# Kernel tuning notes

Hardware: AMD Instinct MI355X
Metric: run time of the kernel (lower is better)

## Reference

```python
import jax, jax.numpy as jnp
import numpy as np

B, T, C, H, HS, L, V, BITS = 4, 512, 768, 12, 64, 12, 50257, 16


def _ln(x, g, b, eps=1e-5):
    m = x.mean(-1, keepdims=True)
    v = ((x - m) ** 2).mean(-1, keepdims=True)
    return (x - m) * jax.lax.rsqrt(v + eps) * g + b


def setup_inputs() -> dict:
    key = jax.random.key(0)
    ks = jax.random.split(key, 12)
    s = 0.02
    return {
        "idx": jax.random.randint(ks[0], (B, T), 0, V),
        "tok_emb": jax.random.normal(ks[1], (V, C), jnp.float32) * s,
        "pos_emb": jax.random.normal(ks[2], (T, C), jnp.float32) * s,
        "Wq": jax.random.normal(ks[3], (L, H, C, HS), jnp.float32) * s,
        "Wk": jax.random.normal(ks[4], (L, H, C, HS), jnp.float32) * s,
        "Wv": jax.random.normal(ks[5], (L, H, C, HS), jnp.float32) * s,
        "Wo": jax.random.normal(ks[6], (L, C, C), jnp.float32) * s,
        "bo": jnp.zeros((L, C), jnp.float32),
        "W1": jax.random.normal(ks[7], (L, C, 4 * C), jnp.float32) * s,
        "b1": jnp.zeros((L, 4 * C), jnp.float32),
        "W2": jax.random.normal(ks[8], (L, 4 * C, C), jnp.float32) * s,
        "b2": jnp.zeros((L, C), jnp.float32),
        "ln1_g": jnp.ones((L, C), jnp.float32),
        "ln1_b": jnp.zeros((L, C), jnp.float32),
        "ln2_g": jnp.ones((L, C), jnp.float32),
        "ln2_b": jnp.zeros((L, C), jnp.float32),
        "lnf_g": jnp.ones((C,), jnp.float32),
        "lnf_b": jnp.zeros((C,), jnp.float32),
        "Wh": jax.random.normal(ks[9], (C, BITS), jnp.float32) * s,
        "bh": jnp.zeros((BITS,), jnp.float32),
    }


def reference(idx, tok_emb, pos_emb, Wq, Wk, Wv, Wo, bo, W1, b1, W2, b2,
              ln1_g, ln1_b, ln2_g, ln2_b, lnf_g, lnf_b, Wh, bh):
    Bc, Tc = idx.shape
    x = tok_emb[idx] + pos_emb[:Tc]          # [B,T,C]
    mask = jnp.tril(jnp.ones((Tc, Tc), bool))  # causal tril buffer
    scale = HS ** -0.5

    def block(x, p):
        wq, wk, wv, wo, bo_, w1, b1_, w2, b2_, g1, bb1, g2, bb2 = p
        xn = _ln(x, g1, bb1)
        q = jnp.einsum('btc,hcd->bhtd', xn, wq)
        k = jnp.einsum('btc,hcd->bhtd', xn, wk)
        v = jnp.einsum('btc,hcd->bhtd', xn, wv)
        wei = jnp.einsum('bhtd,bhsd->bhts', q, k) * scale
        wei = jnp.where(mask, wei, -jnp.inf)
        wei = jax.nn.softmax(wei, axis=-1)
        o = jnp.einsum('bhts,bhsd->bhtd', wei, v)
        o = o.transpose(0, 2, 1, 3).reshape(Bc, Tc, H * HS)  # concat heads
        x = x + o @ wo + bo_
        xn2 = _ln(x, g2, bb2)
        h = jax.nn.gelu(xn2 @ w1 + b1_, approximate=False)  # exact GELU (torch default)
        x = x + h @ w2 + b2_
        return x, None

    x, _ = jax.lax.scan(block, x, (Wq, Wk, Wv, Wo, bo, W1, b1, W2, b2,
                                   ln1_g, ln1_b, ln2_g, ln2_b))
    x = _ln(x, lnf_g, lnf_b)
    logits = x @ Wh + bh                      # [B,T,16] ECOC logits
    return logits
```

## Files before the change

kernel.cpp:

```cpp
#include <hip/hip_runtime.h>
#include <hip/hip_bf16.h>
#include <math.h>

#define TT   512
#define CC   768
#define HH   12
#define HSZ  64
#define LL   12
#define C4   3072
#define BTOT 2048
#define NQKV 2304
#define NX   ((long)BTOT * CC)

typedef __attribute__((ext_vector_type(8))) short short8;
typedef __attribute__((ext_vector_type(4))) float f32x4;

__device__ __forceinline__ unsigned short f2b_bits(float f) {
    unsigned u = __float_as_uint(f);
    return (unsigned short)((u + 0x7fffu + ((u >> 16) & 1u)) >> 16);
}
__device__ __forceinline__ float b2f(unsigned short b) {
    return __uint_as_float((unsigned)b << 16);
}

__device__ __forceinline__ void gl_lds16(const void* g, void* l) {
    __builtin_amdgcn_global_load_lds(
        (const __attribute__((address_space(1))) unsigned int*)g,
        (__attribute__((address_space(3))) unsigned int*)l,
        16, 0, 0);
}

__global__ __launch_bounds__(256) void embed_k(const int* __restrict__ idx,
    const float* __restrict__ tok, const float* __restrict__ pos,
    float* __restrict__ x)
{
    int r   = blockIdx.x;
    int tid = threadIdx.x;
    int t   = r & (TT - 1);
    long id = idx[r];
    const float* te = tok + id * (long)CC;
    const float* pe = pos + (long)t * CC;
    float* xr = x + (long)r * CC;
#pragma unroll
    for (int i = 0; i < 3; ++i) {
        int c = tid + i * 256;
        xr[c] = te[c] + pe[c];
    }
}

__global__ __launch_bounds__(256) void ln_b(const float* __restrict__ x,
    const float* __restrict__ g, const float* __restrict__ b,
    __hip_bfloat16* __restrict__ y)
{
    int r = blockIdx.x, tid = threadIdx.x;
    const float* xr = x + (long)r * CC;
    float v[3];
    v[0] = xr[tid]; v[1] = xr[tid + 256]; v[2] = xr[tid + 512];
    float s  = v[0] + v[1] + v[2];
    float sq = v[0]*v[0] + v[1]*v[1] + v[2]*v[2];
#pragma unroll
    for (int off = 32; off > 0; off >>= 1) {
        s  += __shfl_down(s, off);
        sq += __shfl_down(sq, off);
    }
    __shared__ float ss[4], ssq[4];
    int w = tid >> 6;
    if ((tid & 63) == 0) { ss[w] = s; ssq[w] = sq; }
    __syncthreads();
    s  = ss[0] + ss[1] + ss[2] + ss[3];
    sq = ssq[0] + ssq[1] + ssq[2] + ssq[3];
    float mean = s * (1.0f / CC);
    float var  = sq * (1.0f / CC) - mean * mean;
    float rs   = rsqrtf(var + 1e-5f);
    __hip_bfloat16* yr = y + (long)r * CC;
#pragma unroll
    for (int i = 0; i < 3; ++i) {
        int c = tid + i * 256;
        yr[c] = __float2bfloat16((v[i] - mean) * rs * g[c] + b[c]);
    }
}

template <bool DOLN>
__global__ __launch_bounds__(256) void red_ln(float* __restrict__ x,
    const unsigned short* __restrict__ p, const float* __restrict__ bias,
    const float* __restrict__ g, const float* __restrict__ b,
    __hip_bfloat16* __restrict__ y)
{
    int r = blockIdx.x, tid = threadIdx.x;
    float* xr = x + (long)r * CC;
    const unsigned short* pr = p + (long)r * CC;
    float v[3];
#pragma unroll
    for (int i = 0; i < 3; ++i) {
        int c = tid + i * 256;
        float s = xr[c] + bias[c];
        s += b2f(pr[c]);
        s += b2f(pr[c + 1 * NX]);
        s += b2f(pr[c + 2 * NX]);
        s += b2f(pr[c + 3 * NX]);
        xr[c] = s;
        v[i] = s;
    }
    if (!DOLN) return;
    float s  = v[0] + v[1] + v[2];
    float sq = v[0]*v[0] + v[1]*v[1] + v[2]*v[2];
#pragma unroll
    for (int off = 32; off > 0; off >>= 1) {
        s  += __shfl_down(s, off);
        sq += __shfl_down(sq, off);
    }
    __shared__ float ss[4], ssq[4];
    int w = tid >> 6;
    if ((tid & 63) == 0) { ss[w] = s; ssq[w] = sq; }
    __syncthreads();
    s  = ss[0] + ss[1] + ss[2] + ss[3];
    sq = ssq[0] + ssq[1] + ssq[2] + ssq[3];
    float mean = s * (1.0f / CC);
    float var  = sq * (1.0f / CC) - mean * mean;
    float rs   = rsqrtf(var + 1e-5f);
    __hip_bfloat16* yr = y + (long)r * CC;
#pragma unroll
    for (int i = 0; i < 3; ++i) {
        int c = tid + i * 256;
        yr[c] = __float2bfloat16((v[i] - mean) * rs * g[c] + b[c]);
    }
}

__global__ __launch_bounds__(256) void cvtT_k(const float* __restrict__ src,
    __hip_bfloat16* __restrict__ dst, int R, int D, long sSrc, long sDst)
{
    src += (long)blockIdx.z * sSrc;
    dst += (long)blockIdx.z * sDst;
    __shared__ float t[64][65];
    int d0 = blockIdx.x * 64, r0 = blockIdx.y * 64;
    int tid = threadIdx.x;
#pragma unroll
    for (int i = 0; i < 4; ++i) {
        int flat = tid + i * 256;
        int r = flat >> 4, c4 = (flat & 15) * 4;
        float4 v = *(const float4*)&src[(long)(r0 + r) * D + d0 + c4];
        t[r][c4 + 0] = v.x; t[r][c4 + 1] = v.y;
        t[r][c4 + 2] = v.z; t[r][c4 + 3] = v.w;
    }
    __syncthreads();
#pragma unroll
    for (int i = 0; i < 4; ++i) {
        int flat = tid + i * 256;
        int n = flat >> 4, kq = (flat & 15) * 4;
        ushort4 o;
        o.x = f2b_bits(t[kq + 0][n]); o.y = f2b_bits(t[kq + 1][n]);
        o.z = f2b_bits(t[kq + 2][n]); o.w = f2b_bits(t[kq + 3][n]);
        *(ushort4*)&dst[(long)(d0 + n) * R + r0 + kq] = o;
    }
}

__global__ __launch_bounds__(256) void cvt_qkvT(const float* __restrict__ Wq,
    const float* __restrict__ Wk, const float* __restrict__ Wv,
    __hip_bfloat16* __restrict__ out)
{
    int c0 = blockIdx.x * 64;
    int g  = blockIdx.y;
    int l  = blockIdx.z;
    int which = g / 12, h = g % 12;
    const long wAtt = (long)HH * CC * HSZ;
    const float* src = (which == 0 ? Wq : which == 1 ? Wk : Wv)
                       + l * wAtt + (long)h * CC * HSZ;
    __hip_bfloat16* dst = out + (long)l * NQKV * CC + (long)(which * CC + h * HSZ) * CC;
    __shared__ float t[64][65];
    int tid = threadIdx.x;
#pragma unroll
    for (int i = 0; i < 4; ++i) {
        int flat = tid + i * 256;
        int r = flat >> 4, c4 = (flat & 15) * 4;
        float4 v = *(const float4*)&src[(long)(c0 + r) * HSZ + c4];
        t[r][c4 + 0] = v.x; t[r][c4 + 1] = v.y;
        t[r][c4 + 2] = v.z; t[r][c4 + 3] = v.w;
    }
    __syncthreads();
#pragma unroll
    for (int i = 0; i < 4; ++i) {
        int flat = tid + i * 256;
        int n = flat >> 4, kq = (flat & 15) * 4;
        ushort4 o;
        o.x = f2b_bits(t[kq + 0][n]); o.y = f2b_bits(t[kq + 1][n]);
        o.z = f2b_bits(t[kq + 2][n]); o.w = f2b_bits(t[kq + 3][n]);
        *(ushort4*)&dst[(long)n * CC + c0 + kq] = o;
    }
}

template <int EPI>
__global__ __launch_bounds__(256, 3) void gemm_bf16(
    const __hip_bfloat16* __restrict__ A,
    const __hip_bfloat16* __restrict__ BT,
    __hip_bfloat16* __restrict__ Cb, float* __restrict__ Cf,
    const float* __restrict__ bias, __hip_bfloat16* __restrict__ Vt,
    int K, int lda, int ldb, int ldc)
{
    __shared__ short Asm[4][64 * 32];
    __shared__ short Bsm[4][128 * 32];
    const int tid  = threadIdx.x;
    const int lane = tid & 63;
    const int wid  = tid >> 6;
    const int wm = wid >> 1, wn = wid & 1;

    const int gx = gridDim.x;
    const int slice = gx * gridDim.y;
    int flat = blockIdx.y * gx + blockIdx.x;
    int swz  = (flat & 7) * (slice >> 3) + (flat >> 3);
    const int row0 = (swz / gx) * 64, col0 = (swz % gx) * 128;
    const int sk = (EPI == 5) ? blockIdx.z : 0;

    const int gr = tid >> 2;
    const int cb = ((tid & 3) + (tid >> 3)) & 3;
    const int gk = cb * 8;
    const __hip_bfloat16* Ap = A  + (long)(row0 + gr) * lda + sk * K + gk;
    const __hip_bfloat16* Bp = BT + (long)(col0 + gr) * ldb + sk * K + gk;
    const int lofs = wid * 512;

    f32x4 acc[2][4] = {};
    const int fr = lane & 15, g = lane >> 4;

    int offA[2], offB[4];
#pragma unroll
    for (int m = 0; m < 2; ++m) {
        int row = wm * 32 + m * 16 + fr;
        offA[m] = row * 32 + (((g - (row >> 1)) & 3) * 8);
    }
#pragma unroll
    for (int n = 0; n < 4; ++n) {
        int row = wn * 64 + n * 16 + fr;
        offB[n] = row * 32 + (((g - (row >> 1)) & 3) * 8);
    }

#define STAGE(buf)                                                          \
    do {                                                                    \
        gl_lds16(Ap, &Asm[buf][lofs]);                                      \
        gl_lds16(Bp, &Bsm[buf][lofs]);                                      \
        gl_lds16(Bp + (long)64 * ldb, &Bsm[buf][lofs + 64 * 32]);           \
        Ap += 32; Bp += 32;                                                 \
    } while (0)

    STAGE(0); STAGE(1); STAGE(2);

    const int nt = K >> 5;
    for (int t = 0; t < nt; ++t) {
        if (t < nt - 2)       asm volatile("s_waitcnt vmcnt(6)" ::: "memory");
        else if (t == nt - 2) asm volatile("s_waitcnt vmcnt(3)" ::: "memory");
        else                  asm volatile("s_waitcnt vmcnt(0)" ::: "memory");
        __builtin_amdgcn_s_barrier();
        __builtin_amdgcn_sched_barrier(0);
        if (t + 3 < nt) STAGE((t + 3) & 3);

        const int cur = t & 3;
        short8 af[2], bf[4];
#pragma unroll
        for (int m = 0; m < 2; ++m)
            af[m] = *(const short8*)&Asm[cur][offA[m]];
#pragma unroll
        for (int n = 0; n < 4; ++n)
            bf[n] = *(const short8*)&Bsm[cur][offB[n]];
#pragma unroll
        for (int m = 0; m < 2; ++m)
#pragma unroll
            for (int n = 0; n < 4; ++n)
                acc[m][n] = __builtin_amdgcn_mfma_f32_16x16x32_bf16(
                    af[m], bf[n], acc[m][n], 0, 0, 0);
    }
#undef STAGE

    const int fq = lane >> 4;
#pragma unroll
    for (int m = 0; m < 2; ++m) {
        int rbase = row0 + wm * 32 + m * 16 + fq * 4;
#pragma unroll
        for (int n = 0; n < 4; ++n) {
            int col = col0 + wn * 64 + n * 16 + fr;
            if (EPI == 1 && col >= 1536) {
                int hd = col - 1536;
                int b = rbase >> 9, t = rbase & (TT - 1);
                ushort4 o;
                o.x = f2b_bits(acc[m][n][0]); o.y = f2b_bits(acc[m][n][1]);
                o.z = f2b_bits(acc[m][n][2]); o.w = f2b_bits(acc[m][n][3]);
                *(ushort4*)&Vt[((long)(b * HH + (hd >> 6)) * HSZ + (hd & 63)) * TT + t] = o;
                continue;
            }
            float bv = (EPI == 2) ? bias[col] : 0.f;
#pragma unroll
            for (int j = 0; j < 4; ++j) {
                long row = rbase + j;
                float v = acc[m][n][j];
                if (EPI == 1) {
                    Cb[row * ldc + col] = __float2bfloat16(v);
                } else if (EPI == 2) {
                    v += bv;
                    v = 0.5f * v * (1.0f + erff(v * 0.70710678118654752f));
                    Cb[row * ldc + col] = __float2bfloat16(v);
                } else {
                    Cb[(long)sk * NX + row * ldc + col] = __float2bfloat16(v);
                }
            }
        }
    }
}

__global__ __launch_bounds__(64) void attn_mfma(
    const __hip_bfloat16* __restrict__ qkv,
    const __hip_bfloat16* __restrict__ vT,
    __hip_bfloat16* __restrict__ o)
{
    int flat = blockIdx.x + 16 * (blockIdx.y + 12 * blockIdx.z);
    int swz  = (flat & 7) * 96 + (flat >> 3);
    const int qt = swz & 15;
    const int h  = (swz >> 4) % 12;
    const int b  = swz / 192;
    const int lane = threadIdx.x;
    const int t0 = qt * 32;
    const int fr = lane & 15, g = lane >> 4;

    __shared__ unsigned short P_lds[32 * 40];
    __shared__ float corr_lds[32], l_lds[32];

    const long qbaseA = ((long)(b * TT + t0 + fr)) * NQKV + h * HSZ + g * 8;
    const long qbaseB = qbaseA + (long)16 * NQKV;
    short8 qfA0 = *(const short8*)(qkv + qbaseA);
    short8 qfA1 = *(const short8*)(qkv + qbaseA + 32);
    short8 qfB0 = *(const short8*)(qkv + qbaseB);
    short8 qfB1 = *(const short8*)(qkv + qbaseB + 32);

    f32x4 oaccA[4] = {}, oaccB[4] = {};
    float mA = -3.0e38f, lA = 0.f, mB = -3.0e38f, lB = 0.f;
    const int t_laneA = t0 + fr;
    const int t_laneB = t0 + 16 + fr;
    const int smax = t0 + 31;
    const long kcol = CC + h * HSZ + g * 8;
    const long vrow = (((long)(b * HH + h) * HSZ) + fr) * TT + g * 8;

    short8 ka0, ka1, ka2, ka3;
    {
        long kb0 = ((long)(b * TT + fr)) * NQKV + kcol;
        long kb1 = ((long)(b * TT + 16 + fr)) * NQKV + kcol;
        ka0 = *(const short8*)(qkv + kb0);
        ka1 = *(const short8*)(qkv + kb0 + 32);
        ka2 = *(const short8*)(qkv + kb1);
        ka3 = *(const short8*)(qkv + kb1 + 32);
    }

    for (int s0 = 0; s0 <= smax; s0 += 32) {
        f32x4 stA0 = {}, stA1 = {}, stB0 = {}, stB1 = {};
        stA0 = __builtin_amdgcn_mfma_f32_16x16x32_bf16(ka0, qfA0, stA0, 0, 0, 0);
        stA0 = __builtin_amdgcn_mfma_f32_16x16x32_bf16(ka1, qfA1, stA0, 0, 0, 0);
        stA1 = __builtin_amdgcn_mfma_f32_16x16x32_bf16(ka2, qfA0, stA1, 0, 0, 0);
        stA1 = __builtin_amdgcn_mfma_f32_16x16x32_bf16(ka3, qfA1, stA1, 0, 0, 0);
        stB0 = __builtin_amdgcn_mfma_f32_16x16x32_bf16(ka0, qfB0, stB0, 0, 0, 0);
        stB0 = __builtin_amdgcn_mfma_f32_16x16x32_bf16(ka1, qfB1, stB0, 0, 0, 0);
        stB1 = __builtin_amdgcn_mfma_f32_16x16x32_bf16(ka2, qfB0, stB1, 0, 0, 0);
        stB1 = __builtin_amdgcn_mfma_f32_16x16x32_bf16(ka3, qfB1, stB1, 0, 0, 0);

        const bool more = (s0 + 32 <= smax);
        short8 kn0, kn1, kn2, kn3;
        if (more) {
            long kb0 = ((long)(b * TT + s0 + 32 + fr)) * NQKV + kcol;
            long kb1 = ((long)(b * TT + s0 + 48 + fr)) * NQKV + kcol;
            kn0 = *(const short8*)(qkv + kb0);
            kn1 = *(const short8*)(qkv + kb0 + 32);
            kn2 = *(const short8*)(qkv + kb1);
            kn3 = *(const short8*)(qkv + kb1 + 32);
        }
        short8 vc0 = *(const short8*)(vT + vrow + s0);
        short8 vc1 = *(const short8*)(vT + vrow + 16 * TT + s0);
        short8 vc2 = *(const short8*)(vT + vrow + 32 * TT + s0);
        short8 vc3 = *(const short8*)(vT + vrow + 48 * TT + s0);

        float pA[8];
        float mxA = -3.0e38f;
#pragma unroll
        for (int j = 0; j < 4; ++j) {
            int s = s0 + g * 4 + j;
            float v = stA0[j] * 0.125f;
            v = (s <= t_laneA) ? v : -3.0e38f;
            pA[j] = v; mxA = fmaxf(mxA, v);
        }
#pragma unroll
        for (int j = 0; j < 4; ++j) {
            int s = s0 + 16 + g * 4 + j;
            float v = stA1[j] * 0.125f;
            v = (s <= t_laneA) ? v : -3.0e38f;
            pA[4 + j] = v; mxA = fmaxf(mxA, v);
        }
        mxA = fmaxf(mxA, __shfl_xor(mxA, 16));
        mxA = fmaxf(mxA, __shfl_xor(mxA, 32));
        float mnewA = fmaxf(mA, mxA);
        float corrA = __expf(mA - mnewA);
        float psA = 0.f;
#pragma unroll
        for (int i = 0; i < 8; ++i) {
            float e = __expf(pA[i] - mnewA);
            pA[i] = e; psA += e;
        }
        psA += __shfl_xor(psA, 16);
        psA += __shfl_xor(psA, 32);
        lA = lA * corrA + psA;
        mA = mnewA;

        float pB[8];
        float mxB = -3.0e38f;
#pragma unroll
        for (int j = 0; j < 4; ++j) {
            int s = s0 + g * 4 + j;
            float v = stB0[j] * 0.125f;
            v = (s <= t_laneB) ? v : -3.0e38f;
            pB[j] = v; mxB = fmaxf(mxB, v);
        }
#pragma unroll
        for (int j = 0; j < 4; ++j) {
            int s = s0 + 16 + g * 4 + j;
            float v = stB1[j] * 0.125f;
            v = (s <= t_laneB) ? v : -3.0e38f;
            pB[4 + j] = v; mxB = fmaxf(mxB, v);
        }
        mxB = fmaxf(mxB, __shfl_xor(mxB, 16));
        mxB = fmaxf(mxB, __shfl_xor(mxB, 32));
        float mnewB = fmaxf(mB, mxB);
        float corrB = __expf(mB - mnewB);
        float psB = 0.f;
#pragma unroll
        for (int i = 0; i < 8; ++i) {
            float e = __expf(pB[i] - mnewB);
            pB[i] = e; psB += e;
        }
        psB += __shfl_xor(psB, 16);
        psB += __shfl_xor(psB, 32);
        lB = lB * corrB + psB;
        mB = mnewB;

        if (lane < 16) { corr_lds[lane] = corrA; corr_lds[16 + lane] = corrB; }
        {
            unsigned u0 = (unsigned)f2b_bits(pA[0]) | ((unsigned)f2b_bits(pA[1]) << 16);
            unsigned u1 = (unsigned)f2b_bits(pA[2]) | ((unsigned)f2b_bits(pA[3]) << 16);
            unsigned u2 = (unsigned)f2b_bits(pA[4]) | ((unsigned)f2b_bits(pA[5]) << 16);
            unsigned u3 = (unsigned)f2b_bits(pA[6]) | ((unsigned)f2b_bits(pA[7]) << 16);
            *(unsigned*)&P_lds[fr * 40 + g * 4]          = u0;
            *(unsigned*)&P_lds[fr * 40 + g * 4 + 2]      = u1;
            *(unsigned*)&P_lds[fr * 40 + 16 + g * 4]     = u2;
            *(unsigned*)&P_lds[fr * 40 + 16 + g * 4 + 2] = u3;
        }
        {
            unsigned u0 = (unsigned)f2b_bits(pB[0]) | ((unsigned)f2b_bits(pB[1]) << 16);
            unsigned u1 = (unsigned)f2b_bits(pB[2]) | ((unsigned)f2b_bits(pB[3]) << 16);
            unsigned u2 = (unsigned)f2b_bits(pB[4]) | ((unsigned)f2b_bits(pB[5]) << 16);
            unsigned u3 = (unsigned)f2b_bits(pB[6]) | ((unsigned)f2b_bits(pB[7]) << 16);
            *(unsigned*)&P_lds[(16 + fr) * 40 + g * 4]          = u0;
            *(unsigned*)&P_lds[(16 + fr) * 40 + g * 4 + 2]      = u1;
            *(unsigned*)&P_lds[(16 + fr) * 40 + 16 + g * 4]     = u2;
            *(unsigned*)&P_lds[(16 + fr) * 40 + 16 + g * 4 + 2] = u3;
        }
        __builtin_amdgcn_sched_barrier(0);

        float crA0 = corr_lds[g * 4 + 0], crA1 = corr_lds[g * 4 + 1];
        float crA2 = corr_lds[g * 4 + 2], crA3 = corr_lds[g * 4 + 3];
        float crB0 = corr_lds[16 + g * 4 + 0], crB1 = corr_lds[16 + g * 4 + 1];
        float crB2 = corr_lds[16 + g * 4 + 2], crB3 = corr_lds[16 + g * 4 + 3];
        short8 pfA = *(const short8*)&P_lds[fr * 40 + g * 8];
        short8 pfB = *(const short8*)&P_lds[(16 + fr) * 40 + g * 8];
#pragma unroll
        for (int dt = 0; dt < 4; ++dt) {
            short8 vc = (dt == 0) ? vc0 : (dt == 1) ? vc1 : (dt == 2) ? vc2 : vc3;
            oaccA[dt][0] *= crA0; oaccA[dt][1] *= crA1;
            oaccA[dt][2] *= crA2; oaccA[dt][3] *= crA3;
            oaccA[dt] = __builtin_amdgcn_mfma_f32_16x16x32_bf16(pfA, vc, oaccA[dt], 0, 0, 0);
            oaccB[dt][0] *= crB0; oaccB[dt][1] *= crB1;
            oaccB[dt][2] *= crB2; oaccB[dt][3] *= crB3;
            oaccB[dt] = __builtin_amdgcn_mfma_f32_16x16x32_bf16(pfB, vc, oaccB[dt], 0, 0, 0);
        }

        if (more) { ka0 = kn0; ka1 = kn1; ka2 = kn2; ka3 = kn3; }
        __builtin_amdgcn_sched_barrier(0);
    }

    if (lane < 16) { l_lds[lane] = lA; l_lds[16 + lane] = lB; }
    __builtin_amdgcn_sched_barrier(0);
    float ilA0 = 1.f / l_lds[g * 4 + 0], ilA1 = 1.f / l_lds[g * 4 + 1];
    float ilA2 = 1.f / l_lds[g * 4 + 2], ilA3 = 1.f / l_lds[g * 4 + 3];
    float ilB0 = 1.f / l_lds[16 + g * 4 + 0], ilB1 = 1.f / l_lds[16 + g * 4 + 1];
    float ilB2 = 1.f / l_lds[16 + g * 4 + 2], ilB3 = 1.f / l_lds[16 + g * 4 + 3];
#pragma unroll
    for (int dt = 0; dt < 4; ++dt) {
        long cbaseA = (long)(b * TT + t0) * CC + h * HSZ + dt * 16 + fr;
        long cbaseB = cbaseA + (long)16 * CC;
        o[cbaseA + (g * 4 + 0) * (long)CC] = __float2bfloat16(oaccA[dt][0] * ilA0);
        o[cbaseA + (g * 4 + 1) * (long)CC] = __float2bfloat16(oaccA[dt][1] * ilA1);
        o[cbaseA + (g * 4 + 2) * (long)CC] = __float2bfloat16(oaccA[dt][2] * ilA2);
        o[cbaseA + (g * 4 + 3) * (long)CC] = __float2bfloat16(oaccA[dt][3] * ilA3);
        o[cbaseB + (g * 4 + 0) * (long)CC] = __float2bfloat16(oaccB[dt][0] * ilB0);
        o[cbaseB + (g * 4 + 1) * (long)CC] = __float2bfloat16(oaccB[dt][1] * ilB1);
        o[cbaseB + (g * 4 + 2) * (long)CC] = __float2bfloat16(oaccB[dt][2] * ilB2);
        o[cbaseB + (g * 4 + 3) * (long)CC] = __float2bfloat16(oaccB[dt][3] * ilB3);
    }
}

__global__ __launch_bounds__(256) void head_k(const float* __restrict__ x,
    const float* __restrict__ g, const float* __restrict__ bb,
    const float* __restrict__ Wh, const float* __restrict__ bh,
    float* __restrict__ out)
{
    int r = blockIdx.x, tid = threadIdx.x;
    const float* xr = x + (long)r * CC;
    float v[3];
    v[0] = xr[tid]; v[1] = xr[tid + 256]; v[2] = xr[tid + 512];
    float s  = v[0] + v[1] + v[2];
    float sq = v[0]*v[0] + v[1]*v[1] + v[2]*v[2];
#pragma unroll
    for (int off = 32; off > 0; off >>= 1) {
        s  += __shfl_down(s, off);
        sq += __shfl_down(sq, off);
    }
    __shared__ float ss[4], ssq[4];
    int w = tid >> 6;
    if ((tid & 63) == 0) { ss[w] = s; ssq[w] = sq; }
    __syncthreads();
    s  = ss[0] + ss[1] + ss[2] + ss[3];
    sq = ssq[0] + ssq[1] + ssq[2] + ssq[3];
    float mean = s * (1.0f / CC);
    float var  = sq * (1.0f / CC) - mean * mean;
    float rs   = rsqrtf(var + 1e-5f);

    float acc[16];
#pragma unroll
    for (int j = 0; j < 16; ++j) acc[j] = 0.f;
#pragma unroll
    for (int i = 0; i < 3; ++i) {
        int c = tid + i * 256;
        float xnv = (v[i] - mean) * rs * g[c] + bb[c];
        const float* wr = Wh + (long)c * 16;
#pragma unroll
        for (int j = 0; j < 16; ++j) acc[j] = fmaf(xnv, wr[j], acc[j]);
    }
#pragma unroll
    for (int off = 32; off > 0; off >>= 1)
#pragma unroll
        for (int j = 0; j < 16; ++j) acc[j] += __shfl_down(acc[j], off);
    __shared__ float red[4][16];
    if ((tid & 63) == 0)
#pragma unroll
        for (int j = 0; j < 16; ++j) red[w][j] = acc[j];
    __syncthreads();
    if (tid < 16)
        out[(long)r * 16 + tid] =
            red[0][tid] + red[1][tid] + red[2][tid] + red[3][tid] + bh[tid];
}

extern "C" void kernel_launch(void* const* d_in, const int* in_sizes, int n_in,
                              void* d_out, int out_size, void* d_ws, size_t ws_size,
                              hipStream_t stream)
{
    const int*   idx  = (const int*)  d_in[0];
    const float* tok  = (const float*)d_in[1];
    const float* pos  = (const float*)d_in[2];
    const float* Wq   = (const float*)d_in[3];
    const float* Wk   = (const float*)d_in[4];
    const float* Wv   = (const float*)d_in[5];
    const float* Wo   = (const float*)d_in[6];
    const float* bo   = (const float*)d_in[7];
    const float* W1   = (const float*)d_in[8];
    const float* b1   = (const float*)d_in[9];
    const float* W2   = (const float*)d_in[10];
    const float* b2   = (const float*)d_in[11];
    const float* ln1g = (const float*)d_in[12];
    const float* ln1b = (const float*)d_in[13];
    const float* ln2g = (const float*)d_in[14];
    const float* ln2b = (const float*)d_in[15];
    const float* lnfg = (const float*)d_in[16];
    const float* lnfb = (const float*)d_in[17];
    const float* Wh   = (const float*)d_in[18];
    const float* bh   = (const float*)d_in[19];

    char* w = (char*)d_ws;
    float*          x     = (float*)w;          w += NX * 4;
    __hip_bfloat16* xn_b  = (__hip_bfloat16*)w; w += NX * 2;
    __hip_bfloat16* qkvb  = (__hip_bfloat16*)w; w += (long)BTOT * NQKV * 2;
    __hip_bfloat16* vT    = (__hip_bfloat16*)w; w += NX * 2;
    __hip_bfloat16* o_b   = (__hip_bfloat16*)w; w += NX * 2;
    __hip_bfloat16* hb    = (__hip_bfloat16*)w; w += (long)BTOT * C4 * 2;
    __hip_bfloat16* qkvT  = (__hip_bfloat16*)w; w += (long)LL * NQKV * CC * 2;
    __hip_bfloat16* woT   = (__hip_bfloat16*)w; w += (long)LL * CC * CC * 2;
    __hip_bfloat16* w1T   = (__hip_bfloat16*)w; w += (long)LL * C4 * CC * 2;
    __hip_bfloat16* w2T   = (__hip_bfloat16*)w; w += (long)LL * CC * C4 * 2;
    __hip_bfloat16* pbuf  = (__hip_bfloat16*)w; w += 4 * NX * 2;

    cvt_qkvT<<<dim3(12, 36, LL), 256, 0, stream>>>(Wq, Wk, Wv, qkvT);
    cvtT_k<<<dim3(12, 12, LL), 256, 0, stream>>>(Wo, woT, CC, CC,
        (long)CC * CC, (long)CC * CC);
    cvtT_k<<<dim3(48, 12, LL), 256, 0, stream>>>(W1, w1T, CC, C4,
        (long)CC * C4, (long)CC * C4);
    cvtT_k<<<dim3(12, 48, LL), 256, 0, stream>>>(W2, w2T, C4, CC,
        (long)C4 * CC, (long)C4 * CC);

    embed_k<<<BTOT, 256, 0, stream>>>(idx, tok, pos, x);
    ln_b<<<BTOT, 256, 0, stream>>>(x, ln1g, ln1b, xn_b);

    for (int l = 0; l < LL; ++l) {
        gemm_bf16<1><<<dim3(NQKV / 128, BTOT / 64), 256, 0, stream>>>(
            xn_b, qkvT + (long)l * NQKV * CC, qkvb, nullptr, nullptr, vT,
            CC, CC, CC, NQKV);

        attn_mfma<<<dim3(TT / 32, HH, 4), 64, 0, stream>>>(qkvb, vT, o_b);

        gemm_bf16<5><<<dim3(CC / 128, BTOT / 64, 4), 256, 0, stream>>>(
            o_b, woT + (long)l * CC * CC, pbuf, nullptr, nullptr, nullptr,
            192, CC, CC, CC);

        red_ln<true><<<BTOT, 256, 0, stream>>>(x, (const unsigned short*)pbuf,
            bo + l * CC, ln2g + l * CC, ln2b + l * CC, xn_b);

        gemm_bf16<2><<<dim3(C4 / 128, BTOT / 64), 256, 0, stream>>>(
            xn_b, w1T + (long)l * C4 * CC, hb, nullptr, b1 + l * C4, nullptr,
            CC, CC, CC, C4);

        gemm_bf16<5><<<dim3(CC / 128, BTOT / 64, 4), 256, 0, stream>>>(
            hb, w2T + (long)l * CC * C4, pbuf, nullptr, nullptr, nullptr,
            768, C4, C4, CC);

        if (l < LL - 1) {
            red_ln<true><<<BTOT, 256, 0, stream>>>(x, (const unsigned short*)pbuf,
                b2 + l * CC, ln1g + (l + 1) * CC, ln1b + (l + 1) * CC, xn_b);
        } else {
            red_ln<false><<<BTOT, 256, 0, stream>>>(x, (const unsigned short*)pbuf,
                b2 + l * CC, nullptr, nullptr, nullptr);
        }
    }

    head_k<<<BTOT, 256, 0, stream>>>(x, lnfg, lnfb, Wh, bh, (float*)d_out);
}
```

Measured before the change: 1.382 ms.

## Fuse embed+LN, use tanh GELU, double-buffer attention P, fold final LN

```diff
diff --git a/kernel.cpp b/kernel.cpp
--- a/kernel.cpp
+++ b/kernel.cpp
@@ -22,6 +22,11 @@
 __device__ __forceinline__ float b2f(unsigned short b) {
     return __uint_as_float((unsigned)b << 16);
 }
+__device__ __forceinline__ float gelu_t(float v) {
+    float u = 0.7978845608f * fmaf(0.044715f * v, v * v, v);
+    float th = 1.f - 2.f / (1.f + __expf(2.f * u));
+    return 0.5f * v * (1.f + th);
+}
 
 __device__ __forceinline__ void gl_lds16(const void* g, void* l) {
     __builtin_amdgcn_global_load_lds(
@@ -30,32 +35,24 @@
         16, 0, 0);
 }
 
-__global__ __launch_bounds__(256) void embed_k(const int* __restrict__ idx,
+__global__ __launch_bounds__(256) void embed_ln(const int* __restrict__ idx,
     const float* __restrict__ tok, const float* __restrict__ pos,
-    float* __restrict__ x)
-{
-    int r   = blockIdx.x;
-    int tid = threadIdx.x;
-    int t   = r & (TT - 1);
+    const float* __restrict__ g, const float* __restrict__ b,
+    float* __restrict__ x, __hip_bfloat16* __restrict__ y)
+{
+    int r = blockIdx.x, tid = threadIdx.x;
+    int t = r & (TT - 1);
     long id = idx[r];
     const float* te = tok + id * (long)CC;
     const float* pe = pos + (long)t * CC;
     float* xr = x + (long)r * CC;
+    float v[3];
 #pragma unroll
     for (int i = 0; i < 3; ++i) {
         int c = tid + i * 256;
-        xr[c] = te[c] + pe[c];
-    }
-}
-
-__global__ __launch_bounds__(256) void ln_b(const float* __restrict__ x,
-    const float* __restrict__ g, const float* __restrict__ b,
-    __hip_bfloat16* __restrict__ y)
-{
-    int r = blockIdx.x, tid = threadIdx.x;
-    const float* xr = x + (long)r * CC;
-    float v[3];
-    v[0] = xr[tid]; v[1] = xr[tid + 256]; v[2] = xr[tid + 512];
+        v[i] = te[c] + pe[c];
+        xr[c] = v[i];
+    }
     float s  = v[0] + v[1] + v[2];
     float sq = v[0]*v[0] + v[1]*v[1] + v[2]*v[2];
 #pragma unroll
@@ -292,9 +289,7 @@
                 if (EPI == 1) {
                     Cb[row * ldc + col] = __float2bfloat16(v);
                 } else if (EPI == 2) {
-                    v += bv;
-                    v = 0.5f * v * (1.0f + erff(v * 0.70710678118654752f));
-                    Cb[row * ldc + col] = __float2bfloat16(v);
+                    Cb[row * ldc + col] = __float2bfloat16(gelu_t(v + bv));
                 } else {
                     Cb[(long)sk * NX + row * ldc + col] = __float2bfloat16(v);
                 }
@@ -317,8 +312,8 @@
     const int t0 = qt * 32;
     const int fr = lane & 15, g = lane >> 4;
 
-    __shared__ unsigned short P_lds[32 * 40];
-    __shared__ float corr_lds[32], l_lds[32];
+    __shared__ unsigned short P_lds[2][32 * 40];
+    __shared__ float corr_lds[2][32], l_lds[32];
 
     const long qbaseA = ((long)(b * TT + t0 + fr)) * NQKV + h * HSZ + g * 8;
     const long qbaseB = qbaseA + (long)16 * NQKV;
@@ -346,6 +341,7 @@
     }
 
     for (int s0 = 0; s0 <= smax; s0 += 32) {
+        const int pc = (s0 >> 5) & 1;
         f32x4 stA0 = {}, stA1 = {}, stB0 = {}, stB1 = {};
         stA0 = __builtin_amdgcn_mfma_f32_16x16x32_bf16(ka0, qfA0, stA0, 0, 0, 0);
         stA0 = __builtin_amdgcn_mfma_f32_16x16x32_bf16(ka1, qfA1, stA0, 0, 0, 0);
@@ -433,35 +429,36 @@
         lB = lB * corrB + psB;
         mB = mnewB;
 
-        if (lane < 16) { corr_lds[lane] = corrA; corr_lds[16 + lane] = corrB; }
+        unsigned short* P_w = &P_lds[pc][0];
+        if (lane < 16) { corr_lds[pc][lane] = corrA; corr_lds[pc][16 + lane] = corrB; }
         {
             unsigned u0 = (unsigned)f2b_bits(pA[0]) | ((unsigned)f2b_bits(pA[1]) << 16);
             unsigned u1 = (unsigned)f2b_bits(pA[2]) | ((unsigned)f2b_bits(pA[3]) << 16);
             unsigned u2 = (unsigned)f2b_bits(pA[4]) | ((unsigned)f2b_bits(pA[5]) << 16);
             unsigned u3 = (unsigned)f2b_bits(pA[6]) | ((unsigned)f2b_bits(pA[7]) << 16);
-            *(unsigned*)&P_lds[fr * 40 + g * 4]          = u0;
-            *(unsigned*)&P_lds[fr * 40 + g * 4 + 2]      = u1;
-            *(unsigned*)&P_lds[fr * 40 + 16 + g * 4]     = u2;
-            *(unsigned*)&P_lds[fr * 40 + 16 + g * 4 + 2] = u3;
+            *(unsigned*)&P_w[fr * 40 + g * 4]          = u0;
+            *(unsigned*)&P_w[fr * 40 + g * 4 + 2]      = u1;
+            *(unsigned*)&P_w[fr * 40 + 16 + g * 4]     = u2;
+            *(unsigned*)&P_w[fr * 40 + 16 + g * 4 + 2] = u3;
         }
         {
             unsigned u0 = (unsigned)f2b_bits(pB[0]) | ((unsigned)f2b_bits(pB[1]) << 16);
             unsigned u1 = (unsigned)f2b_bits(pB[2]) | ((unsigned)f2b_bits(pB[3]) << 16);
             unsigned u2 = (unsigned)f2b_bits(pB[4]) | ((unsigned)f2b_bits(pB[5]) << 16);
             unsigned u3 = (unsigned)f2b_bits(pB[6]) | ((unsigned)f2b_bits(pB[7]) << 16);
-            *(unsigned*)&P_lds[(16 + fr) * 40 + g * 4]          = u0;
-            *(unsigned*)&P_lds[(16 + fr) * 40 + g * 4 + 2]      = u1;
-            *(unsigned*)&P_lds[(16 + fr) * 40 + 16 + g * 4]     = u2;
-            *(unsigned*)&P_lds[(16 + fr) * 40 + 16 + g * 4 + 2] = u3;
+            *(unsigned*)&P_w[(16 + fr) * 40 + g * 4]          = u0;
+            *(unsigned*)&P_w[(16 + fr) * 40 + g * 4 + 2]      = u1;
+            *(unsigned*)&P_w[(16 + fr) * 40 + 16 + g * 4]     = u2;
+            *(unsigned*)&P_w[(16 + fr) * 40 + 16 + g * 4 + 2] = u3;
         }
         __builtin_amdgcn_sched_barrier(0);
 
-        float crA0 = corr_lds[g * 4 + 0], crA1 = corr_lds[g * 4 + 1];
-        float crA2 = corr_lds[g * 4 + 2], crA3 = corr_lds[g * 4 + 3];
-        float crB0 = corr_lds[16 + g * 4 + 0], crB1 = corr_lds[16 + g * 4 + 1];
-        float crB2 = corr_lds[16 + g * 4 + 2], crB3 = corr_lds[16 + g * 4 + 3];
-        short8 pfA = *(const short8*)&P_lds[fr * 40 + g * 8];
-        short8 pfB = *(const short8*)&P_lds[(16 + fr) * 40 + g * 8];
+        float crA0 = corr_lds[pc][g * 4 + 0], crA1 = corr_lds[pc][g * 4 + 1];
+        float crA2 = corr_lds[pc][g * 4 + 2], crA3 = corr_lds[pc][g * 4 + 3];
+        float crB0 = corr_lds[pc][16 + g * 4 + 0], crB1 = corr_lds[pc][16 + g * 4 + 1];
+        float crB2 = corr_lds[pc][16 + g * 4 + 2], crB3 = corr_lds[pc][16 + g * 4 + 3];
+        short8 pfA = *(const short8*)&P_w[fr * 40 + g * 8];
+        short8 pfB = *(const short8*)&P_w[(16 + fr) * 40 + g * 8];
 #pragma unroll
         for (int dt = 0; dt < 4; ++dt) {
             short8 vc = (dt == 0) ? vc0 : (dt == 1) ? vc1 : (dt == 2) ? vc2 : vc3;
@@ -474,7 +471,6 @@
         }
 
         if (more) { ka0 = kn0; ka1 = kn1; ka2 = kn2; ka3 = kn3; }
-        __builtin_amdgcn_sched_barrier(0);
     }
 
     if (lane < 16) { l_lds[lane] = lA; l_lds[16 + lane] = lB; }
@@ -498,39 +494,19 @@
     }
 }
 
-__global__ __launch_bounds__(256) void head_k(const float* __restrict__ x,
-    const float* __restrict__ g, const float* __restrict__ bb,
+__global__ __launch_bounds__(256) void head_bf(const __hip_bfloat16* __restrict__ xn,
     const float* __restrict__ Wh, const float* __restrict__ bh,
     float* __restrict__ out)
 {
     int r = blockIdx.x, tid = threadIdx.x;
-    const float* xr = x + (long)r * CC;
-    float v[3];
-    v[0] = xr[tid]; v[1] = xr[tid + 256]; v[2] = xr[tid + 512];
-    float s  = v[0] + v[1] + v[2];
-    float sq = v[0]*v[0] + v[1]*v[1] + v[2]*v[2];
-#pragma unroll
-    for (int off = 32; off > 0; off >>= 1) {
-        s  += __shfl_down(s, off);
-        sq += __shfl_down(sq, off);
-    }
-    __shared__ float ss[4], ssq[4];
-    int w = tid >> 6;
-    if ((tid & 63) == 0) { ss[w] = s; ssq[w] = sq; }
-    __syncthreads();
-    s  = ss[0] + ss[1] + ss[2] + ss[3];
-    sq = ssq[0] + ssq[1] + ssq[2] + ssq[3];
-    float mean = s * (1.0f / CC);
-    float var  = sq * (1.0f / CC) - mean * mean;
-    float rs   = rsqrtf(var + 1e-5f);
-
+    const unsigned short* xr = (const unsigned short*)(xn + (long)r * CC);
     float acc[16];
 #pragma unroll
     for (int j = 0; j < 16; ++j) acc[j] = 0.f;
 #pragma unroll
     for (int i = 0; i < 3; ++i) {
         int c = tid + i * 256;
-        float xnv = (v[i] - mean) * rs * g[c] + bb[c];
+        float xnv = b2f(xr[c]);
         const float* wr = Wh + (long)c * 16;
 #pragma unroll
         for (int j = 0; j < 16; ++j) acc[j] = fmaf(xnv, wr[j], acc[j]);
@@ -540,6 +516,7 @@
 #pragma unroll
         for (int j = 0; j < 16; ++j) acc[j] += __shfl_down(acc[j], off);
     __shared__ float red[4][16];
+    int w = tid >> 6;
     if ((tid & 63) == 0)
 #pragma unroll
         for (int j = 0; j < 16; ++j) red[w][j] = acc[j];
@@ -595,8 +572,7 @@
     cvtT_k<<<dim3(12, 48, LL), 256, 0, stream>>>(W2, w2T, C4, CC,
         (long)C4 * CC, (long)C4 * CC);
 
-    embed_k<<<BTOT, 256, 0, stream>>>(idx, tok, pos, x);
-    ln_b<<<BTOT, 256, 0, stream>>>(x, ln1g, ln1b, xn_b);
+    embed_ln<<<BTOT, 256, 0, stream>>>(idx, tok, pos, ln1g, ln1b, x, xn_b);
 
     for (int l = 0; l < LL; ++l) {
         gemm_bf16<1><<<dim3(NQKV / 128, BTOT / 64), 256, 0, stream>>>(
@@ -620,14 +596,11 @@
             hb, w2T + (long)l * CC * C4, pbuf, nullptr, nullptr, nullptr,
             768, C4, C4, CC);
 
-        if (l < LL - 1) {
-            red_ln<true><<<BTOT, 256, 0, stream>>>(x, (const unsigned short*)pbuf,
-                b2 + l * CC, ln1g + (l + 1) * CC, ln1b + (l + 1) * CC, xn_b);
-        } else {
-            red_ln<false><<<BTOT, 256, 0, stream>>>(x, (const unsigned short*)pbuf,
-                b2 + l * CC, nullptr, nullptr, nullptr);
-        }
-    }
-
-    head_k<<<BTOT, 256, 0, stream>>>(x, lnfg, lnfb, Wh, bh, (float*)d_out);
-}
+        const float* gN = (l < LL - 1) ? (ln1g + (l + 1) * CC) : lnfg;
+        const float* bN = (l < LL - 1) ? (ln1b + (l + 1) * CC) : lnfb;
+        red_ln<true><<<BTOT, 256, 0, stream>>>(x, (const unsigned short*)pbuf,
+            b2 + l * CC, gN, bN, xn_b);
+    }
+
+    head_bf<<<BTOT, 256, 0, stream>>>(xn_b, Wh, bh, (float*)d_out);
+}
```

Result: no change. 1.370 ms (-0.9%).
